# Kernel tuning notes

Hardware: AMD Instinct MI355X
Metric: run time of the kernel (lower is better)

The kernel has to match this reference:

```python
import jax, jax.numpy as jnp
import numpy as np

NUM_ITERATIONS = 10


def _nearest_neighbor(src, tgt):
    # src: [B,N,3], tgt: [B,M,3] -> indices [B,N] of nearest tgt point per src point
    inner = -2.0 * jnp.einsum('bnd,bmd->bnm', src, tgt)            # [B,N,M]
    xx = jnp.sum(src * src, axis=2, keepdims=True)                  # [B,N,1]
    yy = jnp.sum(tgt * tgt, axis=2, keepdims=True).transpose(0, 2, 1)  # [B,1,M]
    distances = xx + inner + yy                                     # [B,N,M]
    return jnp.argmin(distances, axis=2)                            # [B,N]


def _compute_transformation(src, tgt):
    # src, tgt: [B,N,3] matched pairs -> rigid (R [B,3,3], t [B,3])
    N = src.shape[1]
    c_src = jnp.mean(src, axis=1, keepdims=True)                    # [B,1,3]
    c_tgt = jnp.mean(tgt, axis=1, keepdims=True)                    # [B,1,3]
    H = jnp.einsum('bnd,bne->bde', src - c_src, tgt - c_tgt) / N    # [B,3,3]
    U, S, Vh = jnp.linalg.svd(H, full_matrices=False)
    V = jnp.swapaxes(Vh, -1, -2)                                    # matches torch.svd's V
    R = V @ jnp.swapaxes(U, -1, -2)
    det = jnp.linalg.det(R)                                         # [B]
    sign = 1.0 - 2.0 * (det < 0).astype(src.dtype)                  # +1 or -1
    # torch code scales V[:, :, 2] (third column of V)
    V = V * jnp.concatenate([jnp.ones_like(sign)[:, None],
                             jnp.ones_like(sign)[:, None],
                             sign[:, None]], axis=1)[:, None, :]    # scale col 2
    R = V @ jnp.swapaxes(U, -1, -2)                                 # [B,3,3]
    t = c_tgt[:, 0, :] - jnp.einsum('bij,bj->bi', R, c_src[:, 0, :])  # [B,3]
    return R, t


def _icp(src, tgt):
    transformed_src = src
    R = None
    t = None
    for _ in range(NUM_ITERATIONS):
        indices = _nearest_neighbor(transformed_src, tgt)           # [B,N]
        matched_tgt = jnp.take_along_axis(tgt, indices[:, :, None], axis=1)  # [B,N,3]
        R, t = _compute_transformation(transformed_src, matched_tgt)
        # faithful to torch: x @ R + t (R applied on the right)
        transformed_src = jnp.einsum('bnd,bde->bne', transformed_src, R) + t[:, None, :]
    return R, t, transformed_src


def setup_inputs() -> dict:
    key = jax.random.key(0)
    k1, k2 = jax.random.split(key)
    src = jax.random.normal(k1, (4, 4096, 3), dtype=jnp.float32)
    tgt = jax.random.normal(k2, (4, 4096, 3), dtype=jnp.float32)
    return {"src": src, "tgt": tgt}


def reference(src, tgt):
    # Returns (est_R [B,3,3], est_t [B,3], transformed_source [B,N,3])
    return _icp(src, tgt)
```

## Files before the change

kernel.cpp:

```cpp
#include <hip/hip_runtime.h>
#include <math.h>

#define NB 4
#define NP 4096
#define MP 4096

typedef __bf16 bf16x8 __attribute__((ext_vector_type(8)));
typedef float  f32x16 __attribute__((ext_vector_type(16)));

static __device__ __forceinline__ unsigned short bh(float f) {
    unsigned u = __float_as_uint(f);
    unsigned r = (u + 0x7FFFu + ((u >> 16) & 1u)) >> 16;
    return (unsigned short)r;
}
static __device__ __forceinline__ float hf(unsigned short h) {
    return __uint_as_float(((unsigned)h) << 16);
}

__device__ __forceinline__ void kabsch_f32(const float* s, float* RtL) {
    const float invN = 1.0f / (float)NP;
    float cs[3] = { s[0] * invN, s[1] * invN, s[2] * invN };
    float ct[3] = { s[3] * invN, s[4] * invN, s[5] * invN };
    float H[3][3];
    for (int d = 0; d < 3; ++d)
        for (int e = 0; e < 3; ++e)
            H[d][e] = s[6 + d * 3 + e] * invN - cs[d] * ct[e];

    float A[3][3];
    for (int i = 0; i < 3; ++i)
        for (int j = 0; j < 3; ++j)
            A[i][j] = H[0][i] * H[0][j] + H[1][i] * H[1][j] + H[2][i] * H[2][j];

    float V[3][3] = {{1, 0, 0}, {0, 1, 0}, {0, 0, 1}};
    for (int sweep = 0; sweep < 8; ++sweep) {
        float off = A[0][1] * A[0][1] + A[0][2] * A[0][2] + A[1][2] * A[1][2];
        if (off < 1e-16f) break;
        for (int pi = 0; pi < 3; ++pi) {
            const int p = (pi == 2) ? 1 : 0;
            const int q = (pi == 0) ? 1 : 2;
            float apq = A[p][q];
            if (fabsf(apq) < 1e-30f) continue;
            float theta = (A[q][q] - A[p][p]) / (2.0f * apq);
            float t = 1.0f / (fabsf(theta) + sqrtf(1.0f + theta * theta));
            if (theta < 0.0f) t = -t;
            float cth = 1.0f / sqrtf(1.0f + t * t);
            float sth = t * cth;
            float App = A[p][p], Aqq = A[q][q];
            A[p][p] = App - t * apq;
            A[q][q] = Aqq + t * apq;
            A[p][q] = A[q][p] = 0.0f;
            const int r = 3 - p - q;
            float Apr = A[p][r], Aqr = A[q][r];
            A[p][r] = A[r][p] = cth * Apr - sth * Aqr;
            A[q][r] = A[r][q] = sth * Apr + cth * Aqr;
            for (int i = 0; i < 3; ++i) {
                float Vip = V[i][p], Viq = V[i][q];
                V[i][p] = cth * Vip - sth * Viq;
                V[i][q] = sth * Vip + cth * Viq;
            }
        }
    }
    float lam[3] = { A[0][0], A[1][1], A[2][2] };
    for (int i = 0; i < 2; ++i)
        for (int j = i + 1; j < 3; ++j)
            if (lam[j] > lam[i]) {
                float tl = lam[i]; lam[i] = lam[j]; lam[j] = tl;
                for (int k = 0; k < 3; ++k) {
                    float tv = V[k][i]; V[k][i] = V[k][j]; V[k][j] = tv;
                }
            }

    float U[3][3];
    for (int k = 0; k < 3; ++k) {
        float w0 = H[0][0] * V[0][k] + H[0][1] * V[1][k] + H[0][2] * V[2][k];
        float w1 = H[1][0] * V[0][k] + H[1][1] * V[1][k] + H[1][2] * V[2][k];
        float w2 = H[2][0] * V[0][k] + H[2][1] * V[1][k] + H[2][2] * V[2][k];
        float nrm = sqrtf(w0 * w0 + w1 * w1 + w2 * w2);
        if (nrm > 1e-20f) {
            U[0][k] = w0 / nrm; U[1][k] = w1 / nrm; U[2][k] = w2 / nrm;
        } else {
            U[0][k] = U[1][0] * U[2][1] - U[2][0] * U[1][1];
            U[1][k] = U[2][0] * U[0][1] - U[0][0] * U[2][1];
            U[2][k] = U[0][0] * U[1][1] - U[1][0] * U[0][1];
        }
    }

    float detH = H[0][0] * (H[1][1] * H[2][2] - H[1][2] * H[2][1])
               - H[0][1] * (H[1][0] * H[2][2] - H[1][2] * H[2][0])
               + H[0][2] * (H[1][0] * H[2][1] - H[1][1] * H[2][0]);
    float sgn = (detH < 0.0f) ? -1.0f : 1.0f;

    float R[3][3];
    for (int i = 0; i < 3; ++i)
        for (int j = 0; j < 3; ++j)
            R[i][j] = V[i][0] * U[j][0] + V[i][1] * U[j][1] + sgn * V[i][2] * U[j][2];
    float tv[3];
    for (int i = 0; i < 3; ++i)
        tv[i] = ct[i] - (R[i][0] * cs[0] + R[i][1] * cs[1] + R[i][2] * cs[2]);

    for (int i = 0; i < 3; ++i)
        for (int j = 0; j < 3; ++j)
            RtL[i * 3 + j] = R[i][j];
    for (int i = 0; i < 3; ++i) RtL[9 + i] = tv[i];
}

__global__ __launch_bounds__(256) void icp_init(const float* __restrict__ tgt,
                                                float4* __restrict__ tgt4,
                                                uint4* __restrict__ Bbuf) {
    const int t    = blockIdx.x * 256 + threadIdx.x;
    const int b    = t >> 13;
    const int rem  = t & 8191;
    const int tile = rem >> 6;
    const int lane = rem & 63;
    const int n    = lane & 31;
    const int h    = lane >> 5;
    const int gt   = b * MP + tile * 32 + n;

    float x = tgt[gt * 3 + 0];
    float y = tgt[gt * 3 + 1];
    float z = tgt[gt * 3 + 2];
    float wv = x * x + y * y + z * z;

    unsigned short xh = bh(x), xl = bh(x - hf(xh));
    unsigned short yh = bh(y), yl = bh(y - hf(yh));
    unsigned short zh = bh(z), zl = bh(z - hf(zh));
    unsigned short wh = bh(wv), wl = bh(wv - hf(wh));
    const unsigned short ONE = 0x3F80;

    unsigned short s0, s1, s2, s3, s4, s5, s6, s7;
    if (h == 0) { s0 = xh; s1 = xh; s2 = xl; s3 = xl;
                  s4 = yh; s5 = yh; s6 = yl; s7 = yl; }
    else        { s0 = zh; s1 = zh; s2 = zl; s3 = zl;
                  s4 = wh; s5 = wl; s6 = ONE; s7 = ONE; }
    uint4 u;
    u.x = (unsigned)s0 | ((unsigned)s1 << 16);
    u.y = (unsigned)s2 | ((unsigned)s3 << 16);
    u.z = (unsigned)s4 | ((unsigned)s5 << 16);
    u.w = (unsigned)s6 | ((unsigned)s7 << 16);
    Bbuf[t] = u;

    if (h == 0) tgt4[gt] = make_float4(x, y, z, wv);
}

__global__ __launch_bounds__(1024) void icp_scan(
        const float* __restrict__ src,
        const float4* __restrict__ tgt4,
        const uint4* __restrict__ Bbuf,
        float* __restrict__ S,
        const float* __restrict__ pprev,
        float* __restrict__ pout,
        int first) {
    __shared__ unsigned CK[512];
    __shared__ float RtL[12];

    const int blk = blockIdx.x;
    const int b   = blk >> 6;
    const int g   = blk & 63;
    const int tid = threadIdx.x;
    const int w   = tid >> 6;
    const int l   = tid & 63;
    const int ts  = w & 1;
    const int tr  = w >> 1;
    const int gsrc = b * NP + g * 64 + l;

    if (w == 0) {
        if (first) {
            if (l < 12) RtL[l] = (l == 0 || l == 4 || l == 8) ? 1.0f : 0.0f;
        } else {
            const float4* rp = (const float4*)(pprev + (b * 64 + l) * 16);
            float4 r0 = rp[0], r1 = rp[1], r2 = rp[2], r3 = rp[3];
            float sm[15] = { r0.x, r0.y, r0.z, r0.w, r1.x, r1.y, r1.z, r1.w,
                             r2.x, r2.y, r2.z, r2.w, r3.x, r3.y, r3.z };
            #pragma unroll
            for (int k = 0; k < 15; ++k) {
                float v = sm[k];
                v += __shfl_down(v, 32);
                v += __shfl_down(v, 16);
                v += __shfl_down(v, 8);
                v += __shfl_down(v, 4);
                v += __shfl_down(v, 2);
                v += __shfl_down(v, 1);
                sm[k] = v;
            }
            if (l == 0) kabsch_f32(sm, RtL);
        }
    }
    __syncthreads();

    float px, py, pz;
    {
        const float* P = first ? src : S;
        float x = P[gsrc * 3 + 0];
        float y = P[gsrc * 3 + 1];
        float z = P[gsrc * 3 + 2];
        px = x * RtL[0] + y * RtL[3] + z * RtL[6] + RtL[9];
        py = x * RtL[1] + y * RtL[4] + z * RtL[7] + RtL[10];
        pz = x * RtL[2] + y * RtL[5] + z * RtL[8] + RtL[11];
    }
    if (w == 1) {
        S[gsrc * 3 + 0] = px;
        S[gsrc * 3 + 1] = py;
        S[gsrc * 3 + 2] = pz;
    }

    const int h = l >> 5;
    union { unsigned short s[8]; bf16x8 v; } Af;
    {
        const int j3 = ts * 32 + (l & 31);
        float pxj = __shfl(px, j3);
        float pyj = __shfl(py, j3);
        float pzj = __shfl(pz, j3);
        float ax = -2.0f * pxj, ay = -2.0f * pyj, az = -2.0f * pzj;
        float qv = pxj * pxj + pyj * pyj + pzj * pzj + 1.0f;
        unsigned short axh = bh(ax), axl = bh(ax - hf(axh));
        unsigned short ayh = bh(ay), ayl = bh(ay - hf(ayh));
        unsigned short azh = bh(az), azl = bh(az - hf(azh));
        unsigned short qh  = bh(qv), ql  = bh(qv - hf(qh));
        const unsigned short ONE = 0x3F80;
        if (h == 0) {
            Af.s[0] = axh; Af.s[1] = axl; Af.s[2] = axh; Af.s[3] = axl;
            Af.s[4] = ayh; Af.s[5] = ayl; Af.s[6] = ayh; Af.s[7] = ayl;
        } else {
            Af.s[0] = azh; Af.s[1] = azl; Af.s[2] = azh; Af.s[3] = azl;
            Af.s[4] = ONE; Af.s[5] = ONE; Af.s[6] = qh;  Af.s[7] = ql;
        }
    }

    f32x16 zero;
    #pragma unroll
    for (int i = 0; i < 16; ++i) zero[i] = 0.0f;

    float best[16];
    #pragma unroll
    for (int r = 0; r < 16; ++r) best[r] = __uint_as_float(0x7F7FFFFFu);

    const uint4* Bw = Bbuf + (b * 128 + tr * 16) * 64;
    const int col = l & 31;

    uint4 fb[4];
    fb[0] = Bw[l];
    fb[1] = Bw[64 + l];
    fb[2] = Bw[128 + l];
    fb[3] = Bw[192 + l];

    #pragma unroll
    for (int t = 0; t < 16; ++t) {
        bf16x8 Bf = __builtin_bit_cast(bf16x8, fb[t & 3]);
        if (t < 12) fb[t & 3] = Bw[(t + 4) * 64 + l];
        f32x16 d16 = __builtin_amdgcn_mfma_f32_32x32x16_bf16(Af.v, Bf, zero,
                                                             0, 0, 0);
        const unsigned idxk = (unsigned)((tr * 16 + t) * 32 + col);
        #pragma unroll
        for (int r = 0; r < 16; ++r) {
            float key = __uint_as_float(
                (__float_as_uint(d16[r]) & 0xFFFFF000u) | idxk);
            best[r] = fminf(best[r], key);
        }
    }

    #pragma unroll
    for (int r = 0; r < 16; ++r) {
        float v = best[r];
        v = fminf(v, __shfl_xor(v, 1));
        v = fminf(v, __shfl_xor(v, 2));
        v = fminf(v, __shfl_xor(v, 4));
        v = fminf(v, __shfl_xor(v, 8));
        v = fminf(v, __shfl_xor(v, 16));
        best[r] = v;
    }
    if ((l & 31) == 0) {
        #pragma unroll
        for (int r = 0; r < 16; ++r) {
            const int row = (r & 3) + 8 * (r >> 2) + 4 * h;
            CK[tr * 64 + ts * 32 + row] = __float_as_uint(best[r]);
        }
    }
    __syncthreads();

    if (w == 0) {
        unsigned kb = CK[l];
        #pragma unroll
        for (int k = 1; k < 8; ++k) {
            unsigned kk = CK[k * 64 + l];
            kb = kk < kb ? kk : kb;
        }
        const int idx = kb & 0xFFF;
        float4 mt = tgt4[b * MP + idx];
        const float tx = mt.x, ty = mt.y, tz = mt.z;

        float v[15];
        v[0]  = px;      v[1]  = py;      v[2]  = pz;
        v[3]  = tx;      v[4]  = ty;      v[5]  = tz;
        v[6]  = px * tx; v[7]  = px * ty; v[8]  = px * tz;
        v[9]  = py * tx; v[10] = py * ty; v[11] = py * tz;
        v[12] = pz * tx; v[13] = pz * ty; v[14] = pz * tz;
        #pragma unroll
        for (int k = 0; k < 15; ++k) {
            float s = v[k];
            s += __shfl_down(s, 32);
            s += __shfl_down(s, 16);
            s += __shfl_down(s, 8);
            s += __shfl_down(s, 4);
            s += __shfl_down(s, 2);
            s += __shfl_down(s, 1);
            v[k] = s;
        }
        if (l == 0) {
            float* pp = pout + blk * 16;
            #pragma unroll
            for (int k = 0; k < 15; ++k) pp[k] = v[k];
        }
    }
}

__global__ __launch_bounds__(256) void icp_final(
        const float* __restrict__ S,
        const float* __restrict__ plast,
        float* __restrict__ out) {
    __shared__ float RtL[12];
    const int bk  = blockIdx.x;
    const int tid = threadIdx.x;
    const int gid = bk * 256 + tid;
    const int b   = gid >> 12;

    if (tid < 64) {
        const float4* rp = (const float4*)(plast + (b * 64 + tid) * 16);
        float4 r0 = rp[0], r1 = rp[1], r2 = rp[2], r3 = rp[3];
        float sm[15] = { r0.x, r0.y, r0.z, r0.w, r1.x, r1.y, r1.z, r1.w,
                         r2.x, r2.y, r2.z, r2.w, r3.x, r3.y, r3.z };
        #pragma unroll
        for (int k = 0; k < 15; ++k) {
            float v = sm[k];
            v += __shfl_down(v, 32);
            v += __shfl_down(v, 16);
            v += __shfl_down(v, 8);
            v += __shfl_down(v, 4);
            v += __shfl_down(v, 2);
            v += __shfl_down(v, 1);
            sm[k] = v;
        }
        if (tid == 0) kabsch_f32(sm, RtL);
    }
    __syncthreads();

    float x = S[gid * 3 + 0];
    float y = S[gid * 3 + 1];
    float z = S[gid * 3 + 2];
    out[48 + gid * 3 + 0] = x * RtL[0] + y * RtL[3] + z * RtL[6] + RtL[9];
    out[48 + gid * 3 + 1] = x * RtL[1] + y * RtL[4] + z * RtL[7] + RtL[10];
    out[48 + gid * 3 + 2] = x * RtL[2] + y * RtL[5] + z * RtL[8] + RtL[11];
    if ((bk & 15) == 0) {
        if (tid < 9) out[b * 9 + tid] = RtL[tid];
        if (tid < 3) out[36 + b * 3 + tid] = RtL[9 + tid];
    }
}

extern "C" void kernel_launch(void* const* d_in, const int* in_sizes, int n_in,
                              void* d_out, int out_size, void* d_ws, size_t ws_size,
                              hipStream_t stream) {
    const float* src = (const float*)d_in[0];
    const float* tgt = (const float*)d_in[1];
    float* out = (float*)d_out;

    float* W     = (float*)d_ws;
    float4* tgt4 = (float4*)W;
    uint4*  Bbuf = (uint4*)(W + 65536);
    float*  S    = W + 65536 + 131072;
    float*  pA   = S + 49152;
    float*  pB   = pA + 4096;
    float* bufs[2] = { pA, pB };

    icp_init<<<128, 256, 0, stream>>>(tgt, tgt4, Bbuf);
    for (int k = 0; k < 10; ++k) {
        icp_scan<<<256, 1024, 0, stream>>>(src, tgt4, Bbuf, S,
                                           bufs[(k + 1) & 1], bufs[k & 1],
                                           k == 0 ? 1 : 0);
    }
    icp_final<<<64, 256, 0, stream>>>(S, bufs[1], out);
}
```

Measured before the change: 194.0 us.

## Fuse ICP iterations into one cooperative persistent kernel with per-batch atomic barriers

Replaces the ten per-iteration scan launches and the final kernel with one cooperative kernel. Blocks keep their transformed points in registers and wait on per-batch atomic counters for the partial sums from the previous iteration, instead of relying on kernel boundaries. This removes launch overhead and the global round trip of the transformed points. In exchange it relies on all 256 blocks of 1024 threads being co-resident and adds spin-wait latency on the counters.

Measured after the change: 438.2 us. +125.8%, slower.

```diff
diff --git a/kernel.cpp b/kernel.cpp
--- a/kernel.cpp
+++ b/kernel.cpp
@@ -106,8 +106,11 @@
 
 __global__ __launch_bounds__(256) void icp_init(const float* __restrict__ tgt,
                                                 float4* __restrict__ tgt4,
-                                                uint4* __restrict__ Bbuf) {
+                                                uint4* __restrict__ Bbuf,
+                                                unsigned* __restrict__ ctr) {
     const int t    = blockIdx.x * 256 + threadIdx.x;
+    if (t < 40) ctr[t] = 0;
+
     const int b    = t >> 13;
     const int rem  = t & 8191;
     const int tile = rem >> 6;
@@ -142,14 +145,40 @@
     if (h == 0) tgt4[gt] = make_float4(x, y, z, wv);
 }
 
-__global__ __launch_bounds__(1024) void icp_scan(
+__device__ __forceinline__ void solve_rt(const float* __restrict__ pbuf,
+                                         const unsigned* __restrict__ ctr,
+                                         int slot, int b, int l, float* RtL) {
+    const unsigned* cp = &ctr[slot * 4 + b];
+    while (__hip_atomic_load(cp, __ATOMIC_RELAXED, __HIP_MEMORY_SCOPE_AGENT) < 64u)
+        __builtin_amdgcn_s_sleep(2);
+    (void)__hip_atomic_load(cp, __ATOMIC_ACQUIRE, __HIP_MEMORY_SCOPE_AGENT);
+
+    const float4* rp = (const float4*)(pbuf +
+                        ((size_t)(slot * 256 + b * 64 + l)) * 16);
+    float4 r0 = rp[0], r1 = rp[1], r2 = rp[2], r3 = rp[3];
+    float sm[15] = { r0.x, r0.y, r0.z, r0.w, r1.x, r1.y, r1.z, r1.w,
+                     r2.x, r2.y, r2.z, r2.w, r3.x, r3.y, r3.z };
+    #pragma unroll
+    for (int q = 0; q < 15; ++q) {
+        float v = sm[q];
+        v += __shfl_down(v, 32);
+        v += __shfl_down(v, 16);
+        v += __shfl_down(v, 8);
+        v += __shfl_down(v, 4);
+        v += __shfl_down(v, 2);
+        v += __shfl_down(v, 1);
+        sm[q] = v;
+    }
+    if (l == 0) kabsch_f32(sm, RtL);
+}
+
+__global__ __launch_bounds__(1024) void icp_persist(
         const float* __restrict__ src,
         const float4* __restrict__ tgt4,
         const uint4* __restrict__ Bbuf,
-        float* __restrict__ S,
-        const float* __restrict__ pprev,
-        float* __restrict__ pout,
-        int first) {
+        float* __restrict__ pbuf,
+        unsigned* __restrict__ ctr,
+        float* __restrict__ out) {
     __shared__ unsigned CK[512];
     __shared__ float RtL[12];
 
@@ -161,197 +190,154 @@
     const int l   = tid & 63;
     const int ts  = w & 1;
     const int tr  = w >> 1;
+    const int h   = l >> 5;
+    const int col = l & 31;
     const int gsrc = b * NP + g * 64 + l;
 
-    if (w == 0) {
-        if (first) {
-            if (l < 12) RtL[l] = (l == 0 || l == 4 || l == 8) ? 1.0f : 0.0f;
-        } else {
-            const float4* rp = (const float4*)(pprev + (b * 64 + l) * 16);
-            float4 r0 = rp[0], r1 = rp[1], r2 = rp[2], r3 = rp[3];
-            float sm[15] = { r0.x, r0.y, r0.z, r0.w, r1.x, r1.y, r1.z, r1.w,
-                             r2.x, r2.y, r2.z, r2.w, r3.x, r3.y, r3.z };
-            #pragma unroll
-            for (int k = 0; k < 15; ++k) {
-                float v = sm[k];
-                v += __shfl_down(v, 32);
-                v += __shfl_down(v, 16);
-                v += __shfl_down(v, 8);
-                v += __shfl_down(v, 4);
-                v += __shfl_down(v, 2);
-                v += __shfl_down(v, 1);
-                sm[k] = v;
-            }
-            if (l == 0) kabsch_f32(sm, RtL);
-        }
-    }
-    __syncthreads();
-
-    float px, py, pz;
-    {
-        const float* P = first ? src : S;
-        float x = P[gsrc * 3 + 0];
-        float y = P[gsrc * 3 + 1];
-        float z = P[gsrc * 3 + 2];
-        px = x * RtL[0] + y * RtL[3] + z * RtL[6] + RtL[9];
-        py = x * RtL[1] + y * RtL[4] + z * RtL[7] + RtL[10];
-        pz = x * RtL[2] + y * RtL[5] + z * RtL[8] + RtL[11];
-    }
-    if (w == 1) {
-        S[gsrc * 3 + 0] = px;
-        S[gsrc * 3 + 1] = py;
-        S[gsrc * 3 + 2] = pz;
-    }
-
-    const int h = l >> 5;
-    union { unsigned short s[8]; bf16x8 v; } Af;
-    {
-        const int j3 = ts * 32 + (l & 31);
-        float pxj = __shfl(px, j3);
-        float pyj = __shfl(py, j3);
-        float pzj = __shfl(pz, j3);
-        float ax = -2.0f * pxj, ay = -2.0f * pyj, az = -2.0f * pzj;
-        float qv = pxj * pxj + pyj * pyj + pzj * pzj + 1.0f;
-        unsigned short axh = bh(ax), axl = bh(ax - hf(axh));
-        unsigned short ayh = bh(ay), ayl = bh(ay - hf(ayh));
-        unsigned short azh = bh(az), azl = bh(az - hf(azh));
-        unsigned short qh  = bh(qv), ql  = bh(qv - hf(qh));
-        const unsigned short ONE = 0x3F80;
-        if (h == 0) {
-            Af.s[0] = axh; Af.s[1] = axl; Af.s[2] = axh; Af.s[3] = axl;
-            Af.s[4] = ayh; Af.s[5] = ayl; Af.s[6] = ayh; Af.s[7] = ayl;
-        } else {
-            Af.s[0] = azh; Af.s[1] = azl; Af.s[2] = azh; Af.s[3] = azl;
-            Af.s[4] = ONE; Af.s[5] = ONE; Af.s[6] = qh;  Af.s[7] = ql;
-        }
-    }
+    float px = src[gsrc * 3 + 0];
+    float py = src[gsrc * 3 + 1];
+    float pz = src[gsrc * 3 + 2];
+
+    const uint4* Bw = Bbuf + (b * 128 + tr * 16) * 64;
 
     f32x16 zero;
     #pragma unroll
     for (int i = 0; i < 16; ++i) zero[i] = 0.0f;
 
-    float best[16];
-    #pragma unroll
-    for (int r = 0; r < 16; ++r) best[r] = __uint_as_float(0x7F7FFFFFu);
-
-    const uint4* Bw = Bbuf + (b * 128 + tr * 16) * 64;
-    const int col = l & 31;
-
-    uint4 fb[4];
-    fb[0] = Bw[l];
-    fb[1] = Bw[64 + l];
-    fb[2] = Bw[128 + l];
-    fb[3] = Bw[192 + l];
-
-    #pragma unroll
-    for (int t = 0; t < 16; ++t) {
-        bf16x8 Bf = __builtin_bit_cast(bf16x8, fb[t & 3]);
-        if (t < 12) fb[t & 3] = Bw[(t + 4) * 64 + l];
-        f32x16 d16 = __builtin_amdgcn_mfma_f32_32x32x16_bf16(Af.v, Bf, zero,
-                                                             0, 0, 0);
-        const unsigned idxk = (unsigned)((tr * 16 + t) * 32 + col);
+    for (int k = 0; k < 10; ++k) {
+        uint4 fb[4];
+        fb[0] = Bw[l];
+        fb[1] = Bw[64 + l];
+        fb[2] = Bw[128 + l];
+        fb[3] = Bw[192 + l];
+
+        if (w == 0) {
+            if (k == 0) {
+                if (l < 12) RtL[l] = (l == 0 || l == 4 || l == 8) ? 1.0f : 0.0f;
+            } else {
+                solve_rt(pbuf, ctr, k - 1, b, l, RtL);
+            }
+        }
+        __syncthreads();
+
+        {
+            float x = px, y = py, z = pz;
+            px = x * RtL[0] + y * RtL[3] + z * RtL[6] + RtL[9];
+            py = x * RtL[1] + y * RtL[4] + z * RtL[7] + RtL[10];
+            pz = x * RtL[2] + y * RtL[5] + z * RtL[8] + RtL[11];
+        }
+
+        union { unsigned short s[8]; bf16x8 v; } Af;
+        {
+            const int j3 = ts * 32 + (l & 31);
+            float pxj = __shfl(px, j3);
+            float pyj = __shfl(py, j3);
+            float pzj = __shfl(pz, j3);
+            float ax = -2.0f * pxj, ay = -2.0f * pyj, az = -2.0f * pzj;
+            float qv = pxj * pxj + pyj * pyj + pzj * pzj + 1.0f;
+            unsigned short axh = bh(ax), axl = bh(ax - hf(axh));
+            unsigned short ayh = bh(ay), ayl = bh(ay - hf(ayh));
+            unsigned short azh = bh(az), azl = bh(az - hf(azh));
+            unsigned short qh  = bh(qv), ql  = bh(qv - hf(qh));
+            const unsigned short ONE = 0x3F80;
+            if (h == 0) {
+                Af.s[0] = axh; Af.s[1] = axl; Af.s[2] = axh; Af.s[3] = axl;
+                Af.s[4] = ayh; Af.s[5] = ayl; Af.s[6] = ayh; Af.s[7] = ayl;
+            } else {
+                Af.s[0] = azh; Af.s[1] = azl; Af.s[2] = azh; Af.s[3] = azl;
+                Af.s[4] = ONE; Af.s[5] = ONE; Af.s[6] = qh;  Af.s[7] = ql;
+            }
+        }
+
+        float best[16];
+        #pragma unroll
+        for (int r = 0; r < 16; ++r) best[r] = __uint_as_float(0x7F7FFFFFu);
+
+        #pragma unroll
+        for (int t = 0; t < 16; ++t) {
+            bf16x8 Bf = __builtin_bit_cast(bf16x8, fb[t & 3]);
+            if (t < 12) fb[t & 3] = Bw[(t + 4) * 64 + l];
+            f32x16 d16 = __builtin_amdgcn_mfma_f32_32x32x16_bf16(Af.v, Bf, zero,
+                                                                 0, 0, 0);
+            const unsigned idxk = (unsigned)((tr * 16 + t) * 32 + col);
+            #pragma unroll
+            for (int r = 0; r < 16; ++r) {
+                float key = __uint_as_float(
+                    (__float_as_uint(d16[r]) & 0xFFFFF000u) | idxk);
+                best[r] = fminf(best[r], key);
+            }
+        }
+
         #pragma unroll
         for (int r = 0; r < 16; ++r) {
-            float key = __uint_as_float(
-                (__float_as_uint(d16[r]) & 0xFFFFF000u) | idxk);
-            best[r] = fminf(best[r], key);
-        }
-    }
-
-    #pragma unroll
-    for (int r = 0; r < 16; ++r) {
-        float v = best[r];
-        v = fminf(v, __shfl_xor(v, 1));
-        v = fminf(v, __shfl_xor(v, 2));
-        v = fminf(v, __shfl_xor(v, 4));
-        v = fminf(v, __shfl_xor(v, 8));
-        v = fminf(v, __shfl_xor(v, 16));
-        best[r] = v;
-    }
-    if ((l & 31) == 0) {
-        #pragma unroll
-        for (int r = 0; r < 16; ++r) {
-            const int row = (r & 3) + 8 * (r >> 2) + 4 * h;
-            CK[tr * 64 + ts * 32 + row] = __float_as_uint(best[r]);
-        }
-    }
+            float v = best[r];
+            v = fminf(v, __shfl_xor(v, 1));
+            v = fminf(v, __shfl_xor(v, 2));
+            v = fminf(v, __shfl_xor(v, 4));
+            v = fminf(v, __shfl_xor(v, 8));
+            v = fminf(v, __shfl_xor(v, 16));
+            best[r] = v;
+        }
+        if ((l & 31) == 0) {
+            #pragma unroll
+            for (int r = 0; r < 16; ++r) {
+                const int row = (r & 3) + 8 * (r >> 2) + 4 * h;
+                CK[tr * 64 + ts * 32 + row] = __float_as_uint(best[r]);
+            }
+        }
+        __syncthreads();
+
+        if (w == 0) {
+            unsigned kb = CK[l];
+            #pragma unroll
+            for (int q = 1; q < 8; ++q) {
+                unsigned kk = CK[q * 64 + l];
+                kb = kk < kb ? kk : kb;
+            }
+            const int idx = kb & 0xFFF;
+            float4 mt = tgt4[b * MP + idx];
+            const float tx = mt.x, ty = mt.y, tz = mt.z;
+
+            float v[15];
+            v[0]  = px;      v[1]  = py;      v[2]  = pz;
+            v[3]  = tx;      v[4]  = ty;      v[5]  = tz;
+            v[6]  = px * tx; v[7]  = px * ty; v[8]  = px * tz;
+            v[9]  = py * tx; v[10] = py * ty; v[11] = py * tz;
+            v[12] = pz * tx; v[13] = pz * ty; v[14] = pz * tz;
+            #pragma unroll
+            for (int q = 0; q < 15; ++q) {
+                float s = v[q];
+                s += __shfl_down(s, 32);
+                s += __shfl_down(s, 16);
+                s += __shfl_down(s, 8);
+                s += __shfl_down(s, 4);
+                s += __shfl_down(s, 2);
+                s += __shfl_down(s, 1);
+                v[q] = s;
+            }
+            if (l == 0) {
+                float* pp = pbuf + ((size_t)(k * 256 + blk)) * 16;
+                #pragma unroll
+                for (int q = 0; q < 15; ++q)
+                    __hip_atomic_store(&pp[q], v[q], __ATOMIC_RELAXED,
+                                       __HIP_MEMORY_SCOPE_AGENT);
+                __hip_atomic_fetch_add(&ctr[k * 4 + b], 1u, __ATOMIC_RELEASE,
+                                       __HIP_MEMORY_SCOPE_AGENT);
+            }
+        }
+    }
+
+    if (w == 0) solve_rt(pbuf, ctr, 9, b, l, RtL);
     __syncthreads();
 
     if (w == 0) {
-        unsigned kb = CK[l];
-        #pragma unroll
-        for (int k = 1; k < 8; ++k) {
-            unsigned kk = CK[k * 64 + l];
-            kb = kk < kb ? kk : kb;
-        }
-        const int idx = kb & 0xFFF;
-        float4 mt = tgt4[b * MP + idx];
-        const float tx = mt.x, ty = mt.y, tz = mt.z;
-
-        float v[15];
-        v[0]  = px;      v[1]  = py;      v[2]  = pz;
-        v[3]  = tx;      v[4]  = ty;      v[5]  = tz;
-        v[6]  = px * tx; v[7]  = px * ty; v[8]  = px * tz;
-        v[9]  = py * tx; v[10] = py * ty; v[11] = py * tz;
-        v[12] = pz * tx; v[13] = pz * ty; v[14] = pz * tz;
-        #pragma unroll
-        for (int k = 0; k < 15; ++k) {
-            float s = v[k];
-            s += __shfl_down(s, 32);
-            s += __shfl_down(s, 16);
-            s += __shfl_down(s, 8);
-            s += __shfl_down(s, 4);
-            s += __shfl_down(s, 2);
-            s += __shfl_down(s, 1);
-            v[k] = s;
-        }
-        if (l == 0) {
-            float* pp = pout + blk * 16;
-            #pragma unroll
-            for (int k = 0; k < 15; ++k) pp[k] = v[k];
-        }
-    }
-}
-
-__global__ __launch_bounds__(256) void icp_final(
-        const float* __restrict__ S,
-        const float* __restrict__ plast,
-        float* __restrict__ out) {
-    __shared__ float RtL[12];
-    const int bk  = blockIdx.x;
-    const int tid = threadIdx.x;
-    const int gid = bk * 256 + tid;
-    const int b   = gid >> 12;
-
-    if (tid < 64) {
-        const float4* rp = (const float4*)(plast + (b * 64 + tid) * 16);
-        float4 r0 = rp[0], r1 = rp[1], r2 = rp[2], r3 = rp[3];
-        float sm[15] = { r0.x, r0.y, r0.z, r0.w, r1.x, r1.y, r1.z, r1.w,
-                         r2.x, r2.y, r2.z, r2.w, r3.x, r3.y, r3.z };
-        #pragma unroll
-        for (int k = 0; k < 15; ++k) {
-            float v = sm[k];
-            v += __shfl_down(v, 32);
-            v += __shfl_down(v, 16);
-            v += __shfl_down(v, 8);
-            v += __shfl_down(v, 4);
-            v += __shfl_down(v, 2);
-            v += __shfl_down(v, 1);
-            sm[k] = v;
-        }
-        if (tid == 0) kabsch_f32(sm, RtL);
-    }
-    __syncthreads();
-
-    float x = S[gid * 3 + 0];
-    float y = S[gid * 3 + 1];
-    float z = S[gid * 3 + 2];
-    out[48 + gid * 3 + 0] = x * RtL[0] + y * RtL[3] + z * RtL[6] + RtL[9];
-    out[48 + gid * 3 + 1] = x * RtL[1] + y * RtL[4] + z * RtL[7] + RtL[10];
-    out[48 + gid * 3 + 2] = x * RtL[2] + y * RtL[5] + z * RtL[8] + RtL[11];
-    if ((bk & 15) == 0) {
-        if (tid < 9) out[b * 9 + tid] = RtL[tid];
-        if (tid < 3) out[36 + b * 3 + tid] = RtL[9 + tid];
+        float x = px, y = py, z = pz;
+        out[48 + gsrc * 3 + 0] = x * RtL[0] + y * RtL[3] + z * RtL[6] + RtL[9];
+        out[48 + gsrc * 3 + 1] = x * RtL[1] + y * RtL[4] + z * RtL[7] + RtL[10];
+        out[48 + gsrc * 3 + 2] = x * RtL[2] + y * RtL[5] + z * RtL[8] + RtL[11];
+    } else if (w == 1 && g == 0) {
+        if (l < 9) out[b * 9 + l] = RtL[l];
+        if (l < 3) out[36 + b * 3 + l] = RtL[9 + l];
     }
 }
 
@@ -362,19 +348,21 @@
     const float* tgt = (const float*)d_in[1];
     float* out = (float*)d_out;
 
-    float* W     = (float*)d_ws;
-    float4* tgt4 = (float4*)W;
-    uint4*  Bbuf = (uint4*)(W + 65536);
-    float*  S    = W + 65536 + 131072;
-    float*  pA   = S + 49152;
-    float*  pB   = pA + 4096;
-    float* bufs[2] = { pA, pB };
-
-    icp_init<<<128, 256, 0, stream>>>(tgt, tgt4, Bbuf);
-    for (int k = 0; k < 10; ++k) {
-        icp_scan<<<256, 1024, 0, stream>>>(src, tgt4, Bbuf, S,
-                                           bufs[(k + 1) & 1], bufs[k & 1],
-                                           k == 0 ? 1 : 0);
-    }
-    icp_final<<<64, 256, 0, stream>>>(S, bufs[1], out);
-}
+    float* W        = (float*)d_ws;
+    float4* tgt4    = (float4*)W;
+    uint4*  Bbuf    = (uint4*)(W + 65536);
+    float*  pbuf    = W + 65536 + 131072;
+    unsigned* ctr   = (unsigned*)(pbuf + 40960);
+
+    icp_init<<<128, 256, 0, stream>>>(tgt, tgt4, Bbuf, ctr);
+
+    void* args[6];
+    args[0] = (void*)&src;
+    args[1] = (void*)&tgt4;
+    args[2] = (void*)&Bbuf;
+    args[3] = (void*)&pbuf;
+    args[4] = (void*)&ctr;
+    args[5] = (void*)&out;
+    hipLaunchCooperativeKernel((void*)icp_persist, dim3(256), dim3(1024),
+                               args, 0, stream);
+}
```
